# Optimization experiments

Hardware: AMD Instinct MI355X
Metric: run time of the kernel (lower is better)

## Reference

```python
import jax, jax.numpy as jnp
import numpy as np

N_STATES = 64   # n_dice
N_OBS = 128     # number of distinct roll values (rows of log_likelihood table)
T = 262144      # sequence length


def setup_inputs() -> dict:
    key = jax.random.key(0)
    k1, k2, k3 = jax.random.split(key, 3)
    rolls = jax.random.randint(k1, (T,), 0, N_OBS)
    # torch.nn.init.normal(param, -1, 0.1): mean -1, std 0.1
    transition = jax.random.normal(k2, (N_STATES, N_STATES + 1), dtype=jnp.float32) * 0.1 - 1.0
    # emission log-likelihood table [n_obs, n_states]
    loglik_table = jax.nn.log_softmax(
        jax.random.normal(k3, (N_OBS, N_STATES), dtype=jnp.float32), axis=0)
    return {"rolls": rolls, "transition": transition, "loglik_table": loglik_table}


def reference(rolls, transition, loglik_table):
    """Viterbi decode: returns (path, final_score).

    Faithful to CRF.forward / _viterbi_algorithm, including the quirk that the
    emission vector ll_t is added along the PREVIOUS-state axis
    (roll.view(1,-1) broadcast over prev states), and that the returned path is
    in reverse-time order [s_{T-1}, ..., s_0].
    """
    S = transition.shape[0]
    ll = loglik_table[rolls]                 # [T, S]
    trans = transition[:, :S]                # [S, S]  (next, prev)
    init_delta = transition[:, S] + ll[0]    # [S]     start scores

    def step(delta, ll_t):
        # scores[next, prev] = trans[next, prev] + ll_t[prev] + delta[prev]
        scores = trans + (ll_t + delta)[None, :]
        bp = jnp.argmax(scores, axis=1)      # [S] backpointers
        return jnp.max(scores, axis=1), bp

    final_delta, bps = jax.lax.scan(step, init_delta, ll[1:])  # bps: [T-1, S]
    final_state = jnp.argmax(final_delta)
    final_score = final_delta[final_state]

    def back(state, bp_t):
        prev = bp_t[state]
        return prev, prev

    # reverse-time backtrack; ys[t] = decoded state at time t (t = 0..T-2)
    _, ys = jax.lax.scan(back, final_state, bps, reverse=True)
    path = jnp.concatenate([final_state[None], ys[::-1]])  # [s_{T-1},...,s_0]
    return path, final_score
```

## Files before the change

kernel.cpp:

```cpp
#include <hip/hip_runtime.h>
#include <hip/hip_fp16.h>
#include <stdint.h>

#define T_LEN 262144
#define S 64
#define SP1 65

#define L_FWD 32
#define W_FWD 4
#define C_FWD (T_LEN / L_FWD)

#define LB2 8
#define VB2 8
#define NW (T_LEN / LB2)
#define PITCH (LB2 + 2)

template <int CTRL>
__device__ __forceinline__ float dpp_fmax_step(float v) {
    int t = __builtin_amdgcn_update_dpp(__float_as_int(v), __float_as_int(v),
                                        CTRL, 0xf, 0xf, false);
    return fmaxf(__int_as_float(t), v);
}

__device__ __forceinline__ float readlane_f(float v, int lane) {
    return __int_as_float(__builtin_amdgcn_readlane(__float_as_int(v), lane));
}

__device__ __forceinline__ unsigned int pack_key(float a, int j) {
    return (__float_as_uint(a) & 0xFFFFFFC0u) | (unsigned)j;
}

__global__ __launch_bounds__(256, 8) void k1_forward(
    const int* __restrict__ rolls, const float* __restrict__ trans,
    const float* __restrict__ ll,
    unsigned int* __restrict__ bp4, int* __restrict__ wsFinal,
    float* __restrict__ out_score) {
    __shared__ __half strans_h[S * S];
    __shared__ float srowmin[S];
    __shared__ float sMc[S];
    const int tid = threadIdx.x;
    const int lane = tid & 63;
    const int wv = tid >> 6;

    if (blockIdx.x == 0 && tid == 0)
        out_score[0] = 0.0f;

    for (int k = tid; k < S * S; k += 256)
        strans_h[k] = __float2half(trans[(k & 63) * SP1 + (k >> 6)]);
    __syncthreads();

    {
        int i = tid >> 2, q = tid & 3;
        float mn = 3.0e38f;
        #pragma unroll
        for (int u = 0; u < 16; ++u)
            mn = fminf(mn, __half2float(strans_h[((q * 16 + u) << 6) | i]));
        mn = fminf(mn, __shfl_xor(mn, 1));
        mn = fminf(mn, __shfl_xor(mn, 2));
        if (q == 0) srowmin[i] = mn;
    }
    __syncthreads();
    {
        int j = tid >> 2, q = tid & 3;
        float mc = 3.0e38f;
        #pragma unroll
        for (int u = 0; u < 16; ++u) {
            int i = q * 16 + u;
            mc = fminf(mc, srowmin[i] - __half2float(strans_h[(j << 6) | i]));
        }
        mc = fminf(mc, __shfl_xor(mc, 1));
        mc = fminf(mc, __shfl_xor(mc, 2));
        if (q == 0) sMc[j] = mc;
    }
    __syncthreads();
    const float mcol = sMc[lane];

    const int c = blockIdx.x * 4 + wv;
    const int beg_out = c * L_FWD;
    int t0 = beg_out - W_FWD;
    if (t0 < 1) t0 = 1;

    int vroll = rolls[min(t0 + lane, T_LEN - 1)];

    float delta;
    if (c == 0) {
        delta = trans[lane * SP1 + S] + ll[rolls[0] * S + lane];
    } else {
        delta = 0.0f;
    }

    int r0 = __builtin_amdgcn_readlane(vroll, 0);
    int r1 = __builtin_amdgcn_readlane(vroll, 1);
    float ll_cur = ll[r0 * S + lane];
    float ll_nxt = ll[r1 * S + lane];

    int idx = 0;

    auto step = [&]() -> unsigned int {
        int rp = __builtin_amdgcn_readlane(vroll, idx + 2);
        float ll_new = ll[rp * S + lane];

        float cvec = delta + ll_cur;

        float mxc = cvec;
        mxc = dpp_fmax_step<0x111>(mxc);
        mxc = dpp_fmax_step<0x112>(mxc);
        mxc = dpp_fmax_step<0x114>(mxc);
        mxc = dpp_fmax_step<0x118>(mxc);
        mxc = dpp_fmax_step<0x142>(mxc);
        mxc = dpp_fmax_step<0x143>(mxc);
        float cmax = readlane_f(mxc, 63);

        float thr = cmax + mcol;
        unsigned long long mask = __ballot(cvec >= thr);

        int j0 = __ffsll(mask) - 1;
        unsigned long long rm = mask & (mask - 1);
        int j1 = rm ? (__ffsll(rm) - 1) : j0;
        float a0 = __half2float(strans_h[(j0 << 6) | lane]) + readlane_f(cvec, j0);
        float a1 = __half2float(strans_h[(j1 << 6) | lane]) + readlane_f(cvec, j1);
        unsigned int m = min(pack_key(a0, j0), pack_key(a1, j1));

        unsigned long long rest = rm ? (rm & (rm - 1)) : 0ull;
        if (rest) {
            int j2 = __ffsll(rest) - 1;
            unsigned long long r3 = rest & (rest - 1);
            int j3 = r3 ? (__ffsll(r3) - 1) : j2;
            float a2 = __half2float(strans_h[(j2 << 6) | lane]) + readlane_f(cvec, j2);
            float a3 = __half2float(strans_h[(j3 << 6) | lane]) + readlane_f(cvec, j3);
            m = min(m, min(pack_key(a2, j2), pack_key(a3, j3)));
            rest = r3 ? (r3 & (r3 - 1)) : 0ull;
            while (rest) {
                int j = __ffsll(rest) - 1;
                rest &= (rest - 1);
                float a = __half2float(strans_h[(j << 6) | lane]) + readlane_f(cvec, j);
                m = min(m, pack_key(a, j));
            }
        }

        delta = __uint_as_float(m & 0xFFFFFFC0u);
        ll_cur = ll_nxt;
        ll_nxt = ll_new;
        ++idx;
        return m;
    };

    if (c != 0) {
        #pragma unroll
        for (int w = 0; w < W_FWD; ++w)
            (void)step();
    }

    const int qb = beg_out >> 2;
    unsigned int pk[8];
    {
        unsigned int p = 0u;
        int u0 = (c == 0) ? 1 : 0;
        for (int u = u0; u < 4; ++u) {
            unsigned int m = step();
            p = (p >> 8) | ((m & 63u) << 24);
        }
        pk[0] = p;
    }
    #pragma unroll
    for (int q = 1; q < 8; ++q) {
        unsigned int p = 0u;
        #pragma unroll
        for (int u = 0; u < 4; ++u) {
            unsigned int m = step();
            p = (p >> 8) | ((m & 63u) << 24);
        }
        pk[q] = p;
    }
    #pragma unroll
    for (int q = 0; q < 8; ++q)
        bp4[(unsigned)((qb + q) << 6) | (unsigned)lane] = pk[q];

    if (c == C_FWD - 1) {
        float fmx = delta;
        for (int off = 32; off; off >>= 1)
            fmx = fmaxf(fmx, __shfl_xor(fmx, off));
        unsigned long long em = __ballot(delta == fmx);
        if (lane == 0)
            *wsFinal = __ffsll(em) - 1;
    }
}

__global__ __launch_bounds__(256) void k2_backtrack(
    const unsigned int* __restrict__ bp4, const int* __restrict__ wsFinal,
    const int* __restrict__ rolls, const float* __restrict__ trans,
    const float* __restrict__ ll, float* __restrict__ out_path,
    float* __restrict__ out_score) {
    __shared__ int sst[256 * PITCH];
    __shared__ float spart[4];
    const int tid = threadIdx.x;
    const int b = blockIdx.x * 256 + tid;
    const int tlo = b * LB2;
    const int thi = tlo + LB2 - 1;
    int te = thi + VB2;
    int s;
    if (te >= T_LEN - 1) {
        te = T_LEN - 1;
        s = *wsFinal;
    } else {
        s = 0;
    }
    int* row = sst + tid * PITCH;
    #pragma unroll
    for (int u = 0; u < LB2 + VB2 - 1; ++u) {
        int t = te - u;
        if (t > tlo) {
            if (t <= thi + 1) row[t - tlo] = s;
            unsigned int w = bp4[((unsigned)(t >> 2) << 6) | (unsigned)s];
            s = (int)((w >> ((t & 3) << 3)) & 63u);
        }
    }
    row[0] = s;
    __syncthreads();

    #pragma unroll
    for (int u = 0; u < LB2; ++u)
        out_path[T_LEN - 1 - (tlo + u)] = (float)row[u];

    float acc = 0.0f;
    #pragma unroll
    for (int u = 1; u <= LB2; ++u) {
        int t = tlo + u;
        if (t <= T_LEN - 1) {
            int sp = row[u - 1];
            int st = (u == LB2)
                         ? ((tid < 255) ? sst[(tid + 1) * PITCH] : row[LB2])
                         : row[u];
            acc += trans[st * SP1 + sp] + ll[rolls[t] * S + sp];
        }
    }
    if (b == 0) {
        int s0 = row[0];
        acc += trans[s0 * SP1 + S] + ll[rolls[0] * S + s0];
    }

    for (int off = 32; off; off >>= 1)
        acc += __shfl_xor(acc, off);
    if ((tid & 63) == 0) spart[tid >> 6] = acc;
    __syncthreads();
    if (tid == 0)
        atomicAdd(out_score, (spart[0] + spart[1]) + (spart[2] + spart[3]));
}

extern "C" void kernel_launch(void* const* d_in, const int* in_sizes, int n_in,
                              void* d_out, int out_size, void* d_ws, size_t ws_size,
                              hipStream_t stream) {
    const int* rolls = (const int*)d_in[0];
    const float* trans = (const float*)d_in[1];
    const float* ll = (const float*)d_in[2];
    float* out = (float*)d_out;
    char* ws = (char*)d_ws;
    int* wsFinal = (int*)(ws + 8);
    unsigned int* bp4 = (unsigned int*)(ws + 2048);

    k1_forward<<<C_FWD / 4, 256, 0, stream>>>(rolls, trans, ll, bp4, wsFinal,
                                              out + T_LEN);
    k2_backtrack<<<NW / 256, 256, 0, stream>>>(bp4, wsFinal, rolls, trans, ll,
                                               out, out + T_LEN);
}
```

Baseline: 109.0 us.

## Use per-argmax pairwise difference bound table to prune Viterbi candidates

Adds a small precompute kernel that builds a 64x64 table of min over next-states of trans[i,jm]-trans[i,j], rounded down to half. The forward step now finds the argmax lane of cvec through a packed-key DPP min reduction and prunes candidates with a threshold specific to that argmax column, which is tighter than the old global column bound. The argmax candidate is always evaluated, so fewer extra candidates should reach the serial readlane loop. In exchange it costs an extra kernel launch, a 8KB table load into shared memory per block, and a smaller backtrack chunk size (LB2 8->4), which doubles the backtrack thread count.

```diff
diff --git a/kernel.cpp b/kernel.cpp
--- a/kernel.cpp
+++ b/kernel.cpp
@@ -10,10 +10,12 @@
 #define W_FWD 4
 #define C_FWD (T_LEN / L_FWD)
 
-#define LB2 8
+#define LB2 4
 #define VB2 8
 #define NW (T_LEN / LB2)
 #define PITCH (LB2 + 2)
+
+#define WS_D_OFF (2048 + 16 * 1024 * 1024)
 
 template <int CTRL>
 __device__ __forceinline__ float dpp_fmax_step(float v) {
@@ -22,6 +24,13 @@
     return fmaxf(__int_as_float(t), v);
 }
 
+template <int CTRL>
+__device__ __forceinline__ unsigned int dpp_umin_step(unsigned int v) {
+    unsigned int t = (unsigned int)__builtin_amdgcn_update_dpp(
+        (int)v, (int)v, CTRL, 0xf, 0xf, false);
+    return min(t, v);
+}
+
 __device__ __forceinline__ float readlane_f(float v, int lane) {
     return __int_as_float(__builtin_amdgcn_readlane(__float_as_int(v), lane));
 }
@@ -30,14 +39,34 @@
     return (__float_as_uint(a) & 0xFFFFFFC0u) | (unsigned)j;
 }
 
+__global__ __launch_bounds__(256) void k0_mkD(const float* __restrict__ trans,
+                                              __half* __restrict__ Dg) {
+    int p = blockIdx.x * 256 + threadIdx.x;
+    int jm = p >> 6, j = p & 63;
+    float d = 3.0e38f;
+    #pragma unroll 8
+    for (int i = 0; i < S; ++i) {
+        float a = __half2float(__float2half(trans[i * SP1 + jm]));
+        float b = __half2float(__float2half(trans[i * SP1 + j]));
+        d = fminf(d, a - b);
+    }
+    __half h = __float2half(d);
+    if (__half2float(h) > d) {
+        unsigned short u = __half_as_ushort(h);
+        u = (u & 0x8000) ? (unsigned short)(u + 1)
+                         : (u ? (unsigned short)(u - 1) : (unsigned short)0x8001);
+        h = __ushort_as_half(u);
+    }
+    Dg[p] = h;
+}
+
 __global__ __launch_bounds__(256, 8) void k1_forward(
     const int* __restrict__ rolls, const float* __restrict__ trans,
-    const float* __restrict__ ll,
+    const float* __restrict__ ll, const __half* __restrict__ Dg,
     unsigned int* __restrict__ bp4, int* __restrict__ wsFinal,
     float* __restrict__ out_score) {
     __shared__ __half strans_h[S * S];
-    __shared__ float srowmin[S];
-    __shared__ float sMc[S];
+    __shared__ __half sD[S * S];
     const int tid = threadIdx.x;
     const int lane = tid & 63;
     const int wv = tid >> 6;
@@ -47,33 +76,9 @@
 
     for (int k = tid; k < S * S; k += 256)
         strans_h[k] = __float2half(trans[(k & 63) * SP1 + (k >> 6)]);
+    for (int k = tid; k < (S * S) / 2; k += 256)
+        ((unsigned int*)sD)[k] = ((const unsigned int*)Dg)[k];
     __syncthreads();
-
-    {
-        int i = tid >> 2, q = tid & 3;
-        float mn = 3.0e38f;
-        #pragma unroll
-        for (int u = 0; u < 16; ++u)
-            mn = fminf(mn, __half2float(strans_h[((q * 16 + u) << 6) | i]));
-        mn = fminf(mn, __shfl_xor(mn, 1));
-        mn = fminf(mn, __shfl_xor(mn, 2));
-        if (q == 0) srowmin[i] = mn;
-    }
-    __syncthreads();
-    {
-        int j = tid >> 2, q = tid & 3;
-        float mc = 3.0e38f;
-        #pragma unroll
-        for (int u = 0; u < 16; ++u) {
-            int i = q * 16 + u;
-            mc = fminf(mc, srowmin[i] - __half2float(strans_h[(j << 6) | i]));
-        }
-        mc = fminf(mc, __shfl_xor(mc, 1));
-        mc = fminf(mc, __shfl_xor(mc, 2));
-        if (q == 0) sMc[j] = mc;
-    }
-    __syncthreads();
-    const float mcol = sMc[lane];
 
     const int c = blockIdx.x * 4 + wv;
     const int beg_out = c * L_FWD;
@@ -102,38 +107,35 @@
 
         float cvec = delta + ll_cur;
 
-        float mxc = cvec;
-        mxc = dpp_fmax_step<0x111>(mxc);
-        mxc = dpp_fmax_step<0x112>(mxc);
-        mxc = dpp_fmax_step<0x114>(mxc);
-        mxc = dpp_fmax_step<0x118>(mxc);
-        mxc = dpp_fmax_step<0x142>(mxc);
-        mxc = dpp_fmax_step<0x143>(mxc);
-        float cmax = readlane_f(mxc, 63);
-
-        float thr = cmax + mcol;
-        unsigned long long mask = __ballot(cvec >= thr);
-
-        int j0 = __ffsll(mask) - 1;
-        unsigned long long rm = mask & (mask - 1);
-        int j1 = rm ? (__ffsll(rm) - 1) : j0;
-        float a0 = __half2float(strans_h[(j0 << 6) | lane]) + readlane_f(cvec, j0);
-        float a1 = __half2float(strans_h[(j1 << 6) | lane]) + readlane_f(cvec, j1);
-        unsigned int m = min(pack_key(a0, j0), pack_key(a1, j1));
-
-        unsigned long long rest = rm ? (rm & (rm - 1)) : 0ull;
-        if (rest) {
-            int j2 = __ffsll(rest) - 1;
-            unsigned long long r3 = rest & (rest - 1);
-            int j3 = r3 ? (__ffsll(r3) - 1) : j2;
-            float a2 = __half2float(strans_h[(j2 << 6) | lane]) + readlane_f(cvec, j2);
-            float a3 = __half2float(strans_h[(j3 << 6) | lane]) + readlane_f(cvec, j3);
-            m = min(m, min(pack_key(a2, j2), pack_key(a3, j3)));
-            rest = r3 ? (r3 & (r3 - 1)) : 0ull;
-            while (rest) {
-                int j = __ffsll(rest) - 1;
-                rest &= (rest - 1);
-                float a = __half2float(strans_h[(j << 6) | lane]) + readlane_f(cvec, j);
+        unsigned int kv = pack_key(cvec, lane);
+        kv = dpp_umin_step<0x111>(kv);
+        kv = dpp_umin_step<0x112>(kv);
+        kv = dpp_umin_step<0x114>(kv);
+        kv = dpp_umin_step<0x118>(kv);
+        kv = dpp_umin_step<0x142>(kv);
+        kv = dpp_umin_step<0x143>(kv);
+        unsigned int kmin =
+            (unsigned int)__builtin_amdgcn_readlane((int)kv, 63);
+
+        const int jm = (int)(kmin & 63u);
+        float dcol = __half2float(sD[(jm << 6) | lane]);
+        float h0 = __half2float(strans_h[(jm << 6) | lane]);
+        float cjm = readlane_f(cvec, jm);
+        float thr = __uint_as_float(kmin & 0xFFFFFFC0u) + dcol;
+        unsigned int m = pack_key(h0 + cjm, jm);
+
+        unsigned long long mask = __ballot(cvec >= thr) & ~(1ull << jm);
+        if (mask) {
+            int j1 = __ffsll(mask) - 1;
+            unsigned long long rm = mask & (mask - 1);
+            float a1 = __half2float(strans_h[(j1 << 6) | lane]) +
+                       readlane_f(cvec, j1);
+            m = min(m, pack_key(a1, j1));
+            while (rm) {
+                int j = __ffsll(rm) - 1;
+                rm &= (rm - 1);
+                float a = __half2float(strans_h[(j << 6) | lane]) +
+                          readlane_f(cvec, j);
                 m = min(m, pack_key(a, j));
             }
         }
@@ -257,9 +259,11 @@
     char* ws = (char*)d_ws;
     int* wsFinal = (int*)(ws + 8);
     unsigned int* bp4 = (unsigned int*)(ws + 2048);
-
-    k1_forward<<<C_FWD / 4, 256, 0, stream>>>(rolls, trans, ll, bp4, wsFinal,
-                                              out + T_LEN);
+    __half* Dg = (__half*)(ws + WS_D_OFF);
+
+    k0_mkD<<<16, 256, 0, stream>>>(trans, Dg);
+    k1_forward<<<C_FWD / 4, 256, 0, stream>>>(rolls, trans, ll, Dg, bp4,
+                                              wsFinal, out + T_LEN);
     k2_backtrack<<<NW / 256, 256, 0, stream>>>(bp4, wsFinal, rolls, trans, ll,
                                                out, out + T_LEN);
 }
```

New measurement: 116.7 us. +7.0%, slower.

## Fuse max and argmax via packed-key DPP min; swizzle blocks across XCDs

Applied to the files above, without the earlier changes.

The per-step reduction now runs the DPP tree as an unsigned min over keys packing the score's float bits with the lane index. This yields the best previous state and the threshold base in one reduction, so that candidate is evaluated directly and dropped from the ballot mask. Block indices in both kernels are remapped so each XCD processes a contiguous range of chunks, aiming at better L2 locality for the backpointer buffer. The packed-key min relies on all scores being negative, so the unsigned ordering matches reversed float ordering.

```diff
diff --git a/kernel.cpp b/kernel.cpp
--- a/kernel.cpp
+++ b/kernel.cpp
@@ -9,6 +9,7 @@
 #define L_FWD 32
 #define W_FWD 4
 #define C_FWD (T_LEN / L_FWD)
+#define C_PER_XCD (C_FWD / 8)
 
 #define LB2 8
 #define VB2 8
@@ -16,10 +17,10 @@
 #define PITCH (LB2 + 2)
 
 template <int CTRL>
-__device__ __forceinline__ float dpp_fmax_step(float v) {
-    int t = __builtin_amdgcn_update_dpp(__float_as_int(v), __float_as_int(v),
-                                        CTRL, 0xf, 0xf, false);
-    return fmaxf(__int_as_float(t), v);
+__device__ __forceinline__ unsigned int dpp_umin_step(unsigned int v) {
+    unsigned int t = (unsigned int)__builtin_amdgcn_update_dpp(
+        (int)v, (int)v, CTRL, 0xf, 0xf, false);
+    return min(t, v);
 }
 
 __device__ __forceinline__ float readlane_f(float v, int lane) {
@@ -75,7 +76,7 @@
     __syncthreads();
     const float mcol = sMc[lane];
 
-    const int c = blockIdx.x * 4 + wv;
+    const int c = (blockIdx.x & 7) * C_PER_XCD + (blockIdx.x >> 3) * 4 + wv;
     const int beg_out = c * L_FWD;
     int t0 = beg_out - W_FWD;
     if (t0 < 1) t0 = 1;
@@ -102,38 +103,34 @@
 
         float cvec = delta + ll_cur;
 
-        float mxc = cvec;
-        mxc = dpp_fmax_step<0x111>(mxc);
-        mxc = dpp_fmax_step<0x112>(mxc);
-        mxc = dpp_fmax_step<0x114>(mxc);
-        mxc = dpp_fmax_step<0x118>(mxc);
-        mxc = dpp_fmax_step<0x142>(mxc);
-        mxc = dpp_fmax_step<0x143>(mxc);
-        float cmax = readlane_f(mxc, 63);
-
-        float thr = cmax + mcol;
-        unsigned long long mask = __ballot(cvec >= thr);
-
-        int j0 = __ffsll(mask) - 1;
-        unsigned long long rm = mask & (mask - 1);
-        int j1 = rm ? (__ffsll(rm) - 1) : j0;
-        float a0 = __half2float(strans_h[(j0 << 6) | lane]) + readlane_f(cvec, j0);
-        float a1 = __half2float(strans_h[(j1 << 6) | lane]) + readlane_f(cvec, j1);
-        unsigned int m = min(pack_key(a0, j0), pack_key(a1, j1));
-
-        unsigned long long rest = rm ? (rm & (rm - 1)) : 0ull;
-        if (rest) {
-            int j2 = __ffsll(rest) - 1;
-            unsigned long long r3 = rest & (rest - 1);
-            int j3 = r3 ? (__ffsll(r3) - 1) : j2;
-            float a2 = __half2float(strans_h[(j2 << 6) | lane]) + readlane_f(cvec, j2);
-            float a3 = __half2float(strans_h[(j3 << 6) | lane]) + readlane_f(cvec, j3);
-            m = min(m, min(pack_key(a2, j2), pack_key(a3, j3)));
-            rest = r3 ? (r3 & (r3 - 1)) : 0ull;
-            while (rest) {
-                int j = __ffsll(rest) - 1;
-                rest &= (rest - 1);
-                float a = __half2float(strans_h[(j << 6) | lane]) + readlane_f(cvec, j);
+        unsigned int kv = pack_key(cvec, lane);
+        kv = dpp_umin_step<0x111>(kv);
+        kv = dpp_umin_step<0x112>(kv);
+        kv = dpp_umin_step<0x114>(kv);
+        kv = dpp_umin_step<0x118>(kv);
+        kv = dpp_umin_step<0x142>(kv);
+        kv = dpp_umin_step<0x143>(kv);
+        unsigned int kmin =
+            (unsigned int)__builtin_amdgcn_readlane((int)kv, 63);
+
+        const int jm = (int)(kmin & 63u);
+        float h0 = __half2float(strans_h[(jm << 6) | lane]);
+        float cjm = readlane_f(cvec, jm);
+        float thr = __uint_as_float(kmin & 0xFFFFFFC0u) + mcol;
+        unsigned int m = pack_key(h0 + cjm, jm);
+
+        unsigned long long mask = __ballot(cvec >= thr) & ~(1ull << jm);
+        if (mask) {
+            int j1 = __ffsll(mask) - 1;
+            unsigned long long rm = mask & (mask - 1);
+            float a1 = __half2float(strans_h[(j1 << 6) | lane]) +
+                       readlane_f(cvec, j1);
+            m = min(m, pack_key(a1, j1));
+            while (rm) {
+                int j = __ffsll(rm) - 1;
+                rm &= (rm - 1);
+                float a = __half2float(strans_h[(j << 6) | lane]) +
+                          readlane_f(cvec, j);
                 m = min(m, pack_key(a, j));
             }
         }
@@ -194,7 +191,8 @@
     __shared__ int sst[256 * PITCH];
     __shared__ float spart[4];
     const int tid = threadIdx.x;
-    const int b = blockIdx.x * 256 + tid;
+    const int grp = (blockIdx.x & 7) * 16 + (blockIdx.x >> 3);
+    const int b = grp * 256 + tid;
     const int tlo = b * LB2;
     const int thi = tlo + LB2 - 1;
     int te = thi + VB2;
```

Measured after the change: 112.5 us. 1.03x slower.
